# Kernel tuning notes

Measured on AMD Instinct MI355X. Metric: run time of the kernel, lower is better.

## Reference

```python
import jax, jax.numpy as jnp
import numpy as np

B, N, F_IN, T, K, F_OUT = 16, 1536, 64, 12, 3, 64


def setup_inputs() -> dict:
    key = jax.random.key(0)
    k1, k2, k3, k4 = jax.random.split(key, 4)
    x = jax.random.normal(k1, (B, N, F_IN, T), dtype=jnp.float32)
    spatial_attention = jax.random.uniform(k2, (B, N, N), dtype=jnp.float32)
    # stacked Chebyshev polynomials T_0..T_{K-1}, each (N, N); scaled like
    # normalized-Laplacian polynomials to keep magnitudes sane
    cheb = jax.random.normal(k3, (K, N, N), dtype=jnp.float32) * (1.0 / np.sqrt(N))
    # Theta initialized with torch.rand -> uniform[0,1)
    Theta = jax.random.uniform(k4, (K, F_IN, F_OUT), dtype=jnp.float32)
    return {"x": x, "spatial_attention": spatial_attention, "cheb": cheb, "Theta": Theta}


def reference(x, spatial_attention, cheb, Theta):
    # x: (B, N, F_in, T); spatial_attention: (B, N, N)
    # cheb: (K, N, N); Theta: (K, F_in, F_out)
    # Original per (t, k): ((T_k * At)^T @ x[..., t]) @ Theta_k, summed over k, relu.
    # Vectorized over all timesteps at once; small fixed K loop avoids a
    # (K, B, N, N) intermediate.
    n_cheb = cheb.shape[0]
    acc = jnp.zeros(x.shape[:2] + (Theta.shape[-1], x.shape[-1]), dtype=x.dtype)  # (B,N,F_out,T)
    for k in range(n_cheb):
        t_k_with_at = cheb[k][None, :, :] * spatial_attention          # (B, N, N)
        # transpose over node dims is folded into the einsum: sum over source node n
        rhs = jnp.einsum("bnm,bnft->bmft", t_k_with_at, x)             # (B, N, F_in, T)
        acc = acc + jnp.einsum("bmft,fo->bmot", rhs, Theta[k])         # (B, N, F_out, T)
    return jax.nn.relu(acc)
```

## Files before the change

kernel.cpp:

```cpp
#include <hip/hip_runtime.h>
#include <hip/hip_bf16.h>
#include <stdint.h>


#define B_    16
#define N_    1536
#define FIN_  64
#define T_    12
#define K_    3
#define FOUT_ 64
#define C_    768

typedef float          f32x4 __attribute__((ext_vector_type(4)));
typedef short          s16x8 __attribute__((ext_vector_type(8)));
typedef unsigned short u16x4 __attribute__((ext_vector_type(4)));

__device__ __forceinline__ unsigned short f2bf(float f) {
    unsigned int u = __builtin_bit_cast(unsigned int, f);
    return (unsigned short)((u + 0x8000u) >> 16);
}

__global__ __launch_bounds__(256) void s1_theta(const float* __restrict__ x,
                                                const float* __restrict__ Theta,
                                                unsigned short* __restrict__ Y) {
    int bid = blockIdx.x;
    int oc = bid & 7;
    int nc = (bid >> 3) % 6;
    int k  = (bid / 48) % 3;
    int b  = bid / 144;
    int n  = nc * 256 + threadIdx.x;

    const float* xp = x + (size_t)(b * N_ + n) * (FIN_ * T_);
    const float* th = Theta + (size_t)k * FIN_ * FOUT_ + oc * 8;

    float acc[8][12];
#pragma unroll
    for (int o = 0; o < 8; ++o)
#pragma unroll
        for (int t = 0; t < 12; ++t) acc[o][t] = 0.f;

    for (int f = 0; f < FIN_; ++f) {
        f32x4 x0 = *(const f32x4*)(xp + f * 12);
        f32x4 x1 = *(const f32x4*)(xp + f * 12 + 4);
        f32x4 x2 = *(const f32x4*)(xp + f * 12 + 8);
#pragma unroll
        for (int o = 0; o < 8; ++o) {
            float w = th[f * FOUT_ + o];
#pragma unroll
            for (int t = 0; t < 4; ++t) {
                acc[o][t]     += x0[t] * w;
                acc[o][t + 4] += x1[t] * w;
                acc[o][t + 8] += x2[t] * w;
            }
        }
    }

    unsigned short* yp = Y + (size_t)((b * K_ + k) * C_ + oc * 96) * N_ + n;
#pragma unroll
    for (int o = 0; o < 8; ++o)
#pragma unroll
        for (int t = 0; t < 12; ++t)
            yp[(size_t)(o * 12 + t) * N_] = f2bf(acc[o][t]);
}

__global__ __launch_bounds__(256) void s2_gemm(const float* __restrict__ At,
                                               const float* __restrict__ cheb,
                                               const unsigned short* __restrict__ Y,
                                               float* __restrict__ out) {
    __shared__ __align__(16) unsigned short Alds[128 * 40];
    __shared__ __align__(16) unsigned short Blds[128 * 32];

    int bid = blockIdx.x;
    int mt = bid % 12;
    int ct = (bid / 12) % 6;
    int b  = bid / 72;
    int m0 = mt * 128, c0 = ct * 128;

    int tid  = threadIdx.x;
    int lane = tid & 63, wave = tid >> 6;
    int wr = (wave >> 1) * 64, wc = (wave & 1) * 64;
    int l15 = lane & 15;

    int q = tid & 7, g = tid >> 3;

    const float* cb = cheb + (size_t)(q * 4) * N_ + (m0 + g * 4);
    const float* ab = At + (size_t)b * N_ * N_ + (size_t)(q * 4) * N_ + (m0 + g * 4);
    const unsigned short* yb = Y + (size_t)(b * K_) * (C_ * N_)
                                 + (size_t)(c0 + (tid >> 2)) * N_ + (tid & 3) * 8;

    int awb = g * 320 + q * 8;
    int bwb = (tid >> 2) * 64 + ((((tid & 3) ^ ((tid >> 2) & 3))) << 4);
    int ard = (wr + l15) * 80 + (lane >> 4) * 16;
    int brd = (wc + l15) * 64 + (((lane >> 4) ^ (lane & 3)) << 4);

    f32x4 acc[4][4];
#pragma unroll
    for (int mi = 0; mi < 4; ++mi)
#pragma unroll
        for (int ci = 0; ci < 4; ++ci) acc[mi][ci] = (f32x4)0.f;

    for (int nt = 0; nt < 48; ++nt) {
        for (int k = 0; k < K_; ++k) {
            const float* cbk = cb + (size_t)k * (N_ * N_);
            const unsigned short* ybk = yb + (size_t)k * (C_ * N_);
            f32x4 cv[4], av[4];
#pragma unroll
            for (int j = 0; j < 4; ++j) {
                cv[j] = *(const f32x4*)(cbk + (size_t)j * N_);
                av[j] = *(const f32x4*)(ab  + (size_t)j * N_);
            }
            s16x8 y0 = *(const s16x8*)(ybk);
            s16x8 y1 = *(const s16x8*)(ybk + (size_t)64 * N_);

            __syncthreads();

#pragma unroll
            for (int j = 0; j < 4; ++j) cv[j] *= av[j];
#pragma unroll
            for (int i = 0; i < 4; ++i) {
                u16x4 pk = { f2bf(cv[0][i]), f2bf(cv[1][i]),
                             f2bf(cv[2][i]), f2bf(cv[3][i]) };
                *(u16x4*)((char*)Alds + awb + i * 80) = pk;
            }
            *(s16x8*)((char*)Blds + bwb)        = y0;
            *(s16x8*)((char*)Blds + bwb + 4096) = y1;

            __syncthreads();

            s16x8 af[4], bv[4];
#pragma unroll
            for (int mi = 0; mi < 4; ++mi)
                af[mi] = *(const s16x8*)((const char*)Alds + ard + mi * 1280);
#pragma unroll
            for (int ci = 0; ci < 4; ++ci)
                bv[ci] = *(const s16x8*)((const char*)Blds + brd + ci * 1024);
#pragma unroll
            for (int mi = 0; mi < 4; ++mi)
#pragma unroll
                for (int ci = 0; ci < 4; ++ci)
                    acc[mi][ci] = __builtin_amdgcn_mfma_f32_16x16x32_bf16(
                        af[mi], bv[ci], acc[mi][ci], 0, 0, 0);
        }
        cb += 32 * N_;
        ab += 32 * N_;
        yb += 32;
    }

    int rbase = (lane >> 4) * 4;
#pragma unroll
    for (int mi = 0; mi < 4; ++mi) {
#pragma unroll
        for (int ci = 0; ci < 4; ++ci) {
            int m = m0 + wr + mi * 16 + rbase;
            int c = c0 + wc + ci * 16 + l15;
            float* op = out + (size_t)(b * N_ + m) * C_ + c;
#pragma unroll
            for (int r = 0; r < 4; ++r) {
                float v = acc[mi][ci][r];
                op[(size_t)r * C_] = v > 0.f ? v : 0.f;
            }
        }
    }
}

extern "C" void kernel_launch(void* const* d_in, const int* in_sizes, int n_in,
                              void* d_out, int out_size, void* d_ws, size_t ws_size,
                              hipStream_t stream) {
    const float* x    = (const float*)d_in[0];
    const float* At   = (const float*)d_in[1];
    const float* cheb = (const float*)d_in[2];
    const float* Th   = (const float*)d_in[3];
    unsigned short* Y = (unsigned short*)d_ws;
    float* out = (float*)d_out;

    s1_theta<<<dim3(B_ * K_ * 6 * 8), dim3(256), 0, stream>>>(x, Th, Y);
    s2_gemm <<<dim3(B_ * 12 * 6),     dim3(256), 0, stream>>>(At, cheb, Y, out);
}
```

Measured before the change: 1.167 ms.

## Double-buffer LDS and register-prefetch in GEMM, restage theta kernel via LDS

The GEMM kernel now keeps two LDS buffers and two register sets. The next (nt,k) tile's global loads are issued before the barrier, so the memory latency overlaps the MFMA work, and there is one barrier per step instead of two. Block indices are remapped so that neighbouring blocks land on different XCDs. The theta kernel stages 16 nodes of x in LDS and computes all K at once, so each x element is read only once. The cost is higher register pressure, which launch_bounds(256,2) tries to cap.

```diff
diff --git a/kernel.cpp b/kernel.cpp
--- a/kernel.cpp
+++ b/kernel.cpp
@@ -23,57 +23,80 @@
 __global__ __launch_bounds__(256) void s1_theta(const float* __restrict__ x,
                                                 const float* __restrict__ Theta,
                                                 unsigned short* __restrict__ Y) {
+    __shared__ __align__(16) float xt[16][772];
+
     int bid = blockIdx.x;
-    int oc = bid & 7;
-    int nc = (bid >> 3) % 6;
-    int k  = (bid / 48) % 3;
-    int b  = bid / 144;
-    int n  = nc * 256 + threadIdx.x;
-
-    const float* xp = x + (size_t)(b * N_ + n) * (FIN_ * T_);
-    const float* th = Theta + (size_t)k * FIN_ * FOUT_ + oc * 8;
-
-    float acc[8][12];
-#pragma unroll
-    for (int o = 0; o < 8; ++o)
-#pragma unroll
-        for (int t = 0; t < 12; ++t) acc[o][t] = 0.f;
-
-    for (int f = 0; f < FIN_; ++f) {
-        f32x4 x0 = *(const f32x4*)(xp + f * 12);
-        f32x4 x1 = *(const f32x4*)(xp + f * 12 + 4);
-        f32x4 x2 = *(const f32x4*)(xp + f * 12 + 8);
-#pragma unroll
-        for (int o = 0; o < 8; ++o) {
-            float w = th[f * FOUT_ + o];
-#pragma unroll
-            for (int t = 0; t < 4; ++t) {
-                acc[o][t]     += x0[t] * w;
-                acc[o][t + 4] += x1[t] * w;
-                acc[o][t + 8] += x2[t] * w;
+    int nc = bid % 96, b = bid / 96;
+    int n0 = nc * 16;
+    int tid = threadIdx.x;
+
+    const float* xg = x + (size_t)(b * N_ + n0) * 768;
+#pragma unroll
+    for (int i = 0; i < 12; ++i) {
+        int c = i * 256 + tid;
+        int row = c / 192, col = (c % 192) * 4;
+        f32x4 v = *(const f32x4*)(xg + (size_t)c * 4);
+        *(f32x4*)&xt[row][col] = v;
+    }
+    __syncthreads();
+
+    int oo = tid >> 4, nn = tid & 15;
+    const float* th = Theta + oo * 4;
+
+    float acc[3][4][12];
+#pragma unroll
+    for (int k = 0; k < 3; ++k)
+#pragma unroll
+        for (int j = 0; j < 4; ++j)
+#pragma unroll
+            for (int t = 0; t < 12; ++t) acc[k][j][t] = 0.f;
+
+    for (int f = 0; f < 64; ++f) {
+        f32x4 xv0 = *(const f32x4*)&xt[nn][f * 12];
+        f32x4 xv1 = *(const f32x4*)&xt[nn][f * 12 + 4];
+        f32x4 xv2 = *(const f32x4*)&xt[nn][f * 12 + 8];
+#pragma unroll
+        for (int k = 0; k < 3; ++k) {
+            f32x4 tv = *(const f32x4*)(th + (size_t)(k * 64 + f) * 64);
+#pragma unroll
+            for (int j = 0; j < 4; ++j) {
+#pragma unroll
+                for (int t = 0; t < 4; ++t) {
+                    acc[k][j][t]     += tv[j] * xv0[t];
+                    acc[k][j][t + 4] += tv[j] * xv1[t];
+                    acc[k][j][t + 8] += tv[j] * xv2[t];
+                }
             }
         }
     }
 
-    unsigned short* yp = Y + (size_t)((b * K_ + k) * C_ + oc * 96) * N_ + n;
-#pragma unroll
-    for (int o = 0; o < 8; ++o)
-#pragma unroll
-        for (int t = 0; t < 12; ++t)
-            yp[(size_t)(o * 12 + t) * N_] = f2bf(acc[o][t]);
-}
-
-__global__ __launch_bounds__(256) void s2_gemm(const float* __restrict__ At,
-                                               const float* __restrict__ cheb,
-                                               const unsigned short* __restrict__ Y,
-                                               float* __restrict__ out) {
-    __shared__ __align__(16) unsigned short Alds[128 * 40];
-    __shared__ __align__(16) unsigned short Blds[128 * 32];
-
-    int bid = blockIdx.x;
-    int mt = bid % 12;
-    int ct = (bid / 12) % 6;
-    int b  = bid / 72;
+    unsigned short* yp = Y + (size_t)b * (K_ * C_ * (size_t)N_) + n0 + nn;
+#pragma unroll
+    for (int k = 0; k < 3; ++k)
+#pragma unroll
+        for (int j = 0; j < 4; ++j)
+#pragma unroll
+            for (int t = 0; t < 12; ++t) {
+                int c = (oo * 4 + j) * 12 + t;
+                yp[((size_t)k * C_ + c) * N_] = f2bf(acc[k][j][t]);
+            }
+}
+
+#define NN_ ((size_t)N_ * N_)
+#define CN_ ((size_t)C_ * N_)
+
+__global__ __launch_bounds__(256, 2) void s2_gemm(const float* __restrict__ At,
+                                                  const float* __restrict__ cheb,
+                                                  const unsigned short* __restrict__ Y,
+                                                  float* __restrict__ out) {
+    __shared__ __align__(16) unsigned short Alds[2][128 * 40];
+    __shared__ __align__(16) unsigned short Blds[2][128 * 32];
+
+    int hb = blockIdx.x;
+    int lb = (hb & 7) * 144 + (hb >> 3);
+    int mt = lb % 12;
+    int ct = (lb / 12) % 6;
+    int b  = lb / 72;
     int m0 = mt * 128, c0 = ct * 128;
 
     int tid  = threadIdx.x;
@@ -84,12 +107,12 @@
     int q = tid & 7, g = tid >> 3;
 
     const float* cb = cheb + (size_t)(q * 4) * N_ + (m0 + g * 4);
-    const float* ab = At + (size_t)b * N_ * N_ + (size_t)(q * 4) * N_ + (m0 + g * 4);
-    const unsigned short* yb = Y + (size_t)(b * K_) * (C_ * N_)
+    const float* ab = At + (size_t)b * NN_ + (size_t)(q * 4) * N_ + (m0 + g * 4);
+    const unsigned short* yb = Y + (size_t)(b * K_) * CN_
                                  + (size_t)(c0 + (tid >> 2)) * N_ + (tid & 3) * 8;
 
     int awb = g * 320 + q * 8;
-    int bwb = (tid >> 2) * 64 + ((((tid & 3) ^ ((tid >> 2) & 3))) << 4);
+    int bwb = (tid >> 2) * 64 + (((tid & 3) ^ ((tid >> 2) & 3)) << 4);
     int ard = (wr + l15) * 80 + (lane >> 4) * 16;
     int brd = (wc + l15) * 64 + (((lane >> 4) ^ (lane & 3)) << 4);
 
@@ -99,52 +122,61 @@
 #pragma unroll
         for (int ci = 0; ci < 4; ++ci) acc[mi][ci] = (f32x4)0.f;
 
-    for (int nt = 0; nt < 48; ++nt) {
-        for (int k = 0; k < K_; ++k) {
-            const float* cbk = cb + (size_t)k * (N_ * N_);
-            const unsigned short* ybk = yb + (size_t)k * (C_ * N_);
-            f32x4 cv[4], av[4];
-#pragma unroll
-            for (int j = 0; j < 4; ++j) {
-                cv[j] = *(const f32x4*)(cbk + (size_t)j * N_);
-                av[j] = *(const f32x4*)(ab  + (size_t)j * N_);
-            }
-            s16x8 y0 = *(const s16x8*)(ybk);
-            s16x8 y1 = *(const s16x8*)(ybk + (size_t)64 * N_);
-
-            __syncthreads();
-
-#pragma unroll
-            for (int j = 0; j < 4; ++j) cv[j] *= av[j];
-#pragma unroll
-            for (int i = 0; i < 4; ++i) {
-                u16x4 pk = { f2bf(cv[0][i]), f2bf(cv[1][i]),
-                             f2bf(cv[2][i]), f2bf(cv[3][i]) };
-                *(u16x4*)((char*)Alds + awb + i * 80) = pk;
-            }
-            *(s16x8*)((char*)Blds + bwb)        = y0;
-            *(s16x8*)((char*)Blds + bwb + 4096) = y1;
-
-            __syncthreads();
-
-            s16x8 af[4], bv[4];
-#pragma unroll
-            for (int mi = 0; mi < 4; ++mi)
-                af[mi] = *(const s16x8*)((const char*)Alds + ard + mi * 1280);
-#pragma unroll
-            for (int ci = 0; ci < 4; ++ci)
-                bv[ci] = *(const s16x8*)((const char*)Blds + brd + ci * 1024);
-#pragma unroll
-            for (int mi = 0; mi < 4; ++mi)
-#pragma unroll
-                for (int ci = 0; ci < 4; ++ci)
-                    acc[mi][ci] = __builtin_amdgcn_mfma_f32_16x16x32_bf16(
-                        af[mi], bv[ci], acc[mi][ci], 0, 0, 0);
-        }
-        cb += 32 * N_;
-        ab += 32 * N_;
-        yb += 32;
-    }
+    f32x4 cvA[4], avA[4]; s16x8 yA0, yA1;
+    f32x4 cvB[4], avB[4]; s16x8 yB0, yB1;
+
+#define PF(CV, AV, Y0v, Y1v, DNT, KC) do {                                   \
+    const float* cbk_ = cb + (size_t)(KC) * NN_ + (size_t)(DNT) * 32 * N_;   \
+    const float* abk_ = ab + (size_t)(DNT) * 32 * N_;                        \
+    const unsigned short* ybk_ = yb + (size_t)(KC) * CN_ + (DNT) * 32;       \
+    _Pragma("unroll") for (int j = 0; j < 4; ++j) {                          \
+        CV[j] = *(const f32x4*)(cbk_ + (size_t)j * N_);                      \
+        AV[j] = *(const f32x4*)(abk_ + (size_t)j * N_); }                    \
+    Y0v = *(const s16x8*)(ybk_);                                             \
+    Y1v = *(const s16x8*)(ybk_ + (size_t)64 * N_); } while (0)
+
+#define STEP(CV, AV, Y0v, Y1v, PCV, PAV, PY0, PY1, P, PDNT, PKC, DOPF) do {  \
+    char* Ab_ = (char*)Alds[P];                                              \
+    char* Bb_ = (char*)Blds[P];                                              \
+    f32x4 w_[4];                                                             \
+    _Pragma("unroll") for (int j = 0; j < 4; ++j) w_[j] = CV[j] * AV[j];     \
+    _Pragma("unroll") for (int i = 0; i < 4; ++i) {                          \
+        u16x4 pk_ = { f2bf(w_[0][i]), f2bf(w_[1][i]),                        \
+                      f2bf(w_[2][i]), f2bf(w_[3][i]) };                      \
+        *(u16x4*)(Ab_ + awb + i * 80) = pk_; }                               \
+    *(s16x8*)(Bb_ + bwb)        = Y0v;                                       \
+    *(s16x8*)(Bb_ + bwb + 4096) = Y1v;                                       \
+    if (DOPF) { PF(PCV, PAV, PY0, PY1, PDNT, PKC); }                         \
+    asm volatile("s_waitcnt lgkmcnt(0)" ::: "memory");                       \
+    __builtin_amdgcn_s_barrier();                                            \
+    __builtin_amdgcn_sched_barrier(0);                                       \
+    s16x8 af_[4], bv_[4];                                                    \
+    _Pragma("unroll") for (int mi = 0; mi < 4; ++mi)                         \
+        af_[mi] = *(const s16x8*)((const char*)Ab_ + ard + mi * 1280);       \
+    _Pragma("unroll") for (int ci = 0; ci < 4; ++ci)                         \
+        bv_[ci] = *(const s16x8*)((const char*)Bb_ + brd + ci * 1024);       \
+    _Pragma("unroll") for (int mi = 0; mi < 4; ++mi)                         \
+        _Pragma("unroll") for (int ci = 0; ci < 4; ++ci)                     \
+            acc[mi][ci] = __builtin_amdgcn_mfma_f32_16x16x32_bf16(           \
+                af_[mi], bv_[ci], acc[mi][ci], 0, 0, 0);                     \
+    } while (0)
+
+    PF(cvA, avA, yA0, yA1, 0, 0);
+
+    for (int it2 = 0; it2 < 24; ++it2) {
+        bool more = (it2 != 23);
+        STEP(cvA, avA, yA0, yA1, cvB, avB, yB0, yB1, 0, 0, 1, true);
+        STEP(cvB, avB, yB0, yB1, cvA, avA, yA0, yA1, 1, 0, 2, true);
+        STEP(cvA, avA, yA0, yA1, cvB, avB, yB0, yB1, 0, 1, 0, true);
+        STEP(cvB, avB, yB0, yB1, cvA, avA, yA0, yA1, 1, 1, 1, true);
+        STEP(cvA, avA, yA0, yA1, cvB, avB, yB0, yB1, 0, 1, 2, true);
+        STEP(cvB, avB, yB0, yB1, cvA, avA, yA0, yA1, 1, 2, 0, more);
+        cb += (size_t)64 * N_;
+        ab += (size_t)64 * N_;
+        yb += 64;
+    }
+#undef PF
+#undef STEP
 
     int rbase = (lane >> 4) * 4;
 #pragma unroll
@@ -173,6 +205,6 @@
     unsigned short* Y = (unsigned short*)d_ws;
     float* out = (float*)d_out;
 
-    s1_theta<<<dim3(B_ * K_ * 6 * 8), dim3(256), 0, stream>>>(x, Th, Y);
-    s2_gemm <<<dim3(B_ * 12 * 6),     dim3(256), 0, stream>>>(At, cheb, Y, out);
-}
+    s1_theta<<<dim3(B_ * 96),     dim3(256), 0, stream>>>(x, Th, Y);
+    s2_gemm <<<dim3(B_ * 12 * 6), dim3(256), 0, stream>>>(At, cheb, Y, out);
+}
```

Measured after the change: 1.037 ms. 11.1% less time.
